# Optimization experiments

Hardware: AMD Instinct MI355X
Metric: run time of the kernel (lower is better)

## Reference

```python
import jax, jax.numpy as jnp
import numpy as np

B, C_IN, H, W = 16, 3, 128, 128
HID = 256      # backbone hidden channels
NC = 21        # num_classes (CRF tag set)
DN = ('NCHW', 'OIHW', 'NCHW')


def setup_inputs() -> dict:
    key = jax.random.key(0)
    ks = jax.random.split(key, 6)
    return {
        "x": jax.random.normal(ks[0], (B, C_IN, H, W), jnp.float32),
        "conv1_w": jax.random.normal(ks[1], (HID, C_IN, 3, 3), jnp.float32) * 0.05,
        "conv1_b": jnp.zeros((HID,), jnp.float32),
        "conv2_w": jax.random.normal(ks[2], (NC, HID, 1, 1), jnp.float32) * 0.05,
        "conv2_b": jnp.zeros((NC,), jnp.float32),
        "start_trans": jax.random.normal(ks[3], (NC,), jnp.float32) * 0.1,
        "end_trans": jax.random.normal(ks[4], (NC,), jnp.float32) * 0.1,
        "trans": jax.random.normal(ks[5], (NC, NC), jnp.float32) * 0.1,
    }


def _backbone(x, w1, b1, w2, b2):
    h = jax.lax.conv_general_dilated(x, w1, (1, 1), 'SAME', dimension_numbers=DN)
    h = jax.nn.relu(h + b1[None, :, None, None])
    out = jax.lax.conv_general_dilated(h, w2, (1, 1), 'SAME', dimension_numbers=DN)
    return out + b2[None, :, None, None]   # [b, NC, H, W]


def _viterbi_decode(emissions, start, end, trans):
    # emissions: [b, L, C]; mask is all-True (as in the module).
    # Forward max-sum recursion (torchcrf _viterbi_decode semantics).
    score0 = emissions[:, 0] + start            # [b, C]

    def fwd(score, emit_t):
        # score[b, prev] + trans[prev, next] + emit_t[b, next] -> [b, prev, next]
        nxt = score[:, :, None] + trans[None, :, :] + emit_t[:, None, :]
        idx = jnp.argmax(nxt, axis=1).astype(jnp.int32)   # backpointers [b, C]
        return jnp.max(nxt, axis=1), idx

    emits = jnp.swapaxes(emissions[:, 1:], 0, 1)          # [L-1, b, C]
    score, hist = jax.lax.scan(fwd, score0, emits)        # hist: [L-1, b, C]
    score = score + end
    last_tag = jnp.argmax(score, axis=1).astype(jnp.int32)  # [b]

    # Backtrack: tag_t = hist[t][b, tag_{t+1}], t = L-2 .. 0
    def bwd(tag_next, idx_t):
        tag_t = jnp.take_along_axis(idx_t, tag_next[:, None], axis=1)[:, 0]
        return tag_t, tag_t

    _, tags_head = jax.lax.scan(bwd, last_tag, hist, reverse=True)  # [L-1, b]
    tags = jnp.concatenate([tags_head, last_tag[None, :]], axis=0)  # [L, b]
    return jnp.swapaxes(tags, 0, 1)                                  # [b, L]


def reference(x, conv1_w, conv1_b, conv2_w, conv2_b, start_trans, end_trans, trans):
    feats = _backbone(x, conv1_w, conv1_b, conv2_w, conv2_b)  # [b, NC, h, w]
    b, c, h, w = feats.shape
    emissions = feats.reshape(b, c, h * w).transpose(0, 2, 1)  # [b, L, C]
    tags = _viterbi_decode(emissions, start_trans, end_trans, trans)  # [b, L]
    return tags.reshape(b, h, w)
```

## Files before the change

kernel.cpp:

```cpp
#include <hip/hip_runtime.h>
#include <stdint.h>

#define NB 16
#define HH 128
#define WW 128
#define L (HH*WW)
#define CIN 3
#define HID 256
#define NC 21
#define CHUNK 256
#define NCHUNKS (L/CHUNK)
#define T_PER 32
#define NPACK (L/4)

__global__ __launch_bounds__(256) void k_conv(
    const float* __restrict__ x, const float* __restrict__ w1,
    const float* __restrict__ b1, const float* __restrict__ w2,
    const float* __restrict__ b2, float* __restrict__ emT)
{
    __shared__ float xs[CIN*4*WW];
    int tid = threadIdx.x;
    int g  = blockIdx.x * 256 + tid;
    int b  = g >> 14;
    int t0 = (blockIdx.x * 256) & (L-1);
    int y0 = t0 >> 7;
    int dy = tid >> 7;
    int xx = tid & (WW-1);
    int t  = t0 + tid;

    const float* xb = x + (size_t)b * CIN * L;
    for (int i = tid; i < CIN*4*WW; i += 256) {
        int ic  = i >> 9;
        int rem = i & 511;
        int rr  = rem >> 7;
        int cc  = rem & 127;
        int row = y0 - 1 + rr;
        xs[i] = (row >= 0 && row < HH) ? xb[ic*L + (row<<7) + cc] : 0.f;
    }
    __syncthreads();

    double p[27];
    #pragma unroll
    for (int ic = 0; ic < CIN; ++ic) {
        #pragma unroll
        for (int ky = 0; ky < 3; ++ky) {
            #pragma unroll
            for (int kx = 0; kx < 3; ++kx) {
                int xc = xx + kx - 1;
                float v = (xc >= 0 && xc < WW) ? xs[ic*512 + (dy+ky)*128 + xc] : 0.f;
                p[ic*9 + ky*3 + kx] = (double)v;
            }
        }
    }

    double acc[NC];
    #pragma unroll
    for (int c = 0; c < NC; ++c) acc[c] = 0.0;

    #pragma unroll 2
    for (int oc = 0; oc < HID; ++oc) {
        double hv = 0.0;
        #pragma unroll
        for (int j = 0; j < 27; ++j) hv += (double)w1[oc*27 + j] * p[j];
        float h32 = (float)hv;
        h32 = h32 + b1[oc];
        h32 = fmaxf(h32, 0.f);
        double hd = (double)h32;
        #pragma unroll
        for (int c = 0; c < NC; ++c) acc[c] += (double)w2[c*HID + oc] * hd;
    }
    float* dstb = emT + (size_t)b * NC * L;
    #pragma unroll
    for (int c = 0; c < NC; ++c) {
        float e32 = (float)acc[c];
        dstb[(size_t)c * L + t] = e32 + b2[c];
    }
}

#define NEGINF (-__builtin_huge_valf())

__global__ __launch_bounds__(64) void k_scores(
    const float* __restrict__ emT, const float* __restrict__ start,
    const float* __restrict__ endt, const float* __restrict__ trans,
    float* __restrict__ sc, int* __restrict__ last_tag)
{
    __shared__ float smem[128];
    __shared__ float fin[NC];
    int l = threadIdx.x;
    int b = blockIdx.x;
    int c = l / 21; if (c > 2) c = 2;
    int n = l - c*21; if (n > 20) n = 20;
    int wb = 8*c;

    const float4* er4 = (const float4*)(emT + ((size_t)b * NC + n) * L);
    float*        scp = sc + (size_t)b * NC * L;

    float tc0, tc1, tc2, tc3, tc4, tc5, tc6, tc7;
    {
        int p0=wb, p1=wb+1, p2=wb+2, p3=wb+3, p4=wb+4, p5=wb+5, p6=wb+6, p7=wb+7;
        tc0 = trans[p0*NC + n];
        tc1 = trans[p1*NC + n];
        tc2 = trans[p2*NC + n];
        tc3 = trans[p3*NC + n];
        tc4 = trans[p4*NC + n];
        tc5 = (p5 < NC) ? trans[p5*NC + n] : NEGINF;
        tc6 = (p6 < NC) ? trans[p6*NC + n] : NEGINF;
        tc7 = (p7 < NC) ? trans[p7*NC + n] : NEGINF;
    }
    asm volatile("" : "+v"(tc0), "+v"(tc1), "+v"(tc2), "+v"(tc3));
    asm volatile("" : "+v"(tc4), "+v"(tc5), "+v"(tc6), "+v"(tc7));

    #define STEP(CUR, NXT, EV, RB) { \
        RB = smem[(CUR)*64 + l];                            \
        smem[(NXT)*64 + l] = NEGINF;                        \
        float4 ra  = *(const float4*)&smem[(CUR)*64 + wb]; \
        float4 rb4 = *(const float4*)&smem[(CUR)*64 + wb + 4]; \
        float w0 = ra.x  + tc0, w1 = ra.y  + tc1, w2 = ra.z  + tc2, w3 = ra.w  + tc3; \
        float w4 = rb4.x + tc4, w5 = rb4.y + tc5, w6 = rb4.z + tc6, w7 = rb4.w + tc7; \
        float m0 = fmaxf(fmaxf(w0, w1), w2); \
        float m1 = fmaxf(fmaxf(w3, w4), w5); \
        float m2 = fmaxf(w6, w7); \
        float q  = fmaxf(fmaxf(m0, m1), m2) + (EV);         \
        (void)__hip_atomic_fetch_max(&smem[(NXT)*64 + n], q, \
                 __ATOMIC_RELAXED, __HIP_MEMORY_SCOPE_WORKGROUP);  \
    }

    float4 ebuf0 = er4[0];
    float4 ebuf1 = er4[1];

    float v0 = ebuf0.x + start[n];
    smem[l] = (l < NC) ? v0 : NEGINF;
    float p0 = v0, p1, p2;
    {
        float4 ev = ebuf0;
        ebuf0 = er4[2];
        float rbB, rbC, rbD;
        STEP(0, 1, ev.y, rbB)
        STEP(1, 0, ev.z, rbC)
        STEP(0, 1, ev.w, rbD)
        (void)rbB;
        p1 = rbC; p2 = rbD;
    }

    for (int k = 1; k < NPACK; ++k) {
        float4 ev = (k & 1) ? ebuf1 : ebuf0;
        int kp = k + 2; if (kp > NPACK-1) kp = NPACK-1;
        if (k & 1) ebuf1 = er4[kp]; else ebuf0 = er4[kp];

        float rbA, rbB, rbC, rbD;
        STEP(1, 0, ev.x, rbA)
        if (l < NC) *(float4*)(scp + (k-1)*84 + n*4) = make_float4(p0, p1, p2, rbA);
        STEP(0, 1, ev.y, rbB)
        STEP(1, 0, ev.z, rbC)
        STEP(0, 1, ev.w, rbD)
        p0 = rbB; p1 = rbC; p2 = rbD;
    }
    #undef STEP

    float slast = smem[64 + l];
    if (l < NC) {
        *(float4*)(scp + (NPACK-1)*84 + n*4) = make_float4(p0, p1, p2, slast);
        fin[n] = slast;
    }
    __syncthreads();
    if (l == 0) {
        float bv = fin[0] + endt[0]; int bt = 0;
        #pragma unroll
        for (int j = 1; j < NC; ++j) {
            float v = fin[j] + endt[j];
            if (v > bv) { bv = v; bt = j; }
        }
        last_tag[b] = bt;
    }
}

__global__ __launch_bounds__(256) void k_bp(
    const float* __restrict__ emT, const float* __restrict__ sc,
    const float* __restrict__ trans, uint8_t* __restrict__ bp)
{
    int wave = threadIdx.x >> 6;
    int lane = threadIdx.x & 63;
    int ne   = lane < NC ? lane : NC-1;

    int bidx  = blockIdx.x;
    int b     = bidx >> 7;
    int tbase = (bidx & 127) * (4*T_PER) + wave*T_PER;

    const float* emb = emT + (size_t)b * NC * L;
    const float* scp = sc  + (size_t)b * NC * L;
    uint8_t*     bpb = bp  + (size_t)b * L * NC;

    float tc[NC];
    #pragma unroll
    for (int pp = 0; pp < NC; ++pp) tc[pp] = trans[pp*NC + ne];

    for (int t = tbase; t < tbase + T_PER; ++t) {
        if (t == 0) continue;
        float target = scp[(t>>2)*84 + ne*4 + (t&3)];
        float e      = emb[(size_t)ne * L + t];
        const float* sp = scp + ((t-1)>>2)*84 + ((t-1)&3);
        int fi = 0;
        #pragma unroll
        for (int pp = NC-1; pp >= 0; --pp) {
            float cand = (sp[pp*4] + tc[pp]) + e;
            if (cand == target) fi = pp;
        }
        if (lane < NC) bpb[(size_t)t * NC + ne] = (uint8_t)fi;
    }
}

__global__ __launch_bounds__(64) void k_jump(
    const uint8_t* __restrict__ bp, uint8_t* __restrict__ J)
{
    __shared__ uint32_t lds4[CHUNK*NC/4];
    __shared__ uint8_t  segJ[8*NC];
    int l   = threadIdx.x;
    int bid = blockIdx.x;
    int b   = bid / (NCHUNKS-1);
    int k   = bid % (NCHUNKS-1) + 1;
    int cs  = k * CHUNK;

    const uint32_t* src = (const uint32_t*)(bp + (size_t)b * L * NC + (size_t)cs * NC);
    for (int i = l; i < CHUNK*NC/4; i += 64) lds4[i] = src[i];
    __syncthreads();
    const uint8_t* lb = (const uint8_t*)lds4;

    int c0 = l, c1 = l + 63, c2 = l + 126;
    bool v2 = (c2 < 8*NC);
    int t0 = c0 % NC, t1 = c1 % NC, t2 = v2 ? (c2 % NC) : 0;
    int r0 = (c0 / NC) * 32, r1 = (c1 / NC) * 32, r2 = v2 ? (c2 / NC) * 32 : 0;
    for (int i = 31; i >= 0; --i) {
        t0 = lb[(r0+i)*NC + t0];
        t1 = lb[(r1+i)*NC + t1];
        if (v2) t2 = lb[(r2+i)*NC + t2];
    }
    segJ[c0] = (uint8_t)t0;
    segJ[c1] = (uint8_t)t1;
    if (v2) segJ[c2] = (uint8_t)t2;
    __syncthreads();

    if (l < NC) {
        int tag = l;
        #pragma unroll
        for (int s = 7; s >= 0; --s) tag = segJ[s*NC + tag];
        J[((size_t)b * NCHUNKS + k) * NC + l] = (uint8_t)tag;
    }
}

__global__ __launch_bounds__(64) void k_seq(
    const uint8_t* __restrict__ J, const int* __restrict__ last_tag,
    uint8_t* __restrict__ ent)
{
    __shared__ uint32_t ldsJ4[NB*NCHUNKS*NC/4];
    int l = threadIdx.x;
    const uint32_t* src = (const uint32_t*)J;
    for (int i = l; i < NB*NCHUNKS*NC/4; i += 64) ldsJ4[i] = src[i];
    __syncthreads();
    const uint8_t* lj = (const uint8_t*)ldsJ4;

    if (l < NB) {
        int b = l;
        int tag = last_tag[b];
        ent[b * NCHUNKS + 63] = (uint8_t)tag;
        for (int k = NCHUNKS-1; k >= 1; --k) {
            tag = lj[((size_t)b * NCHUNKS + k) * NC + tag];
            ent[b * NCHUNKS + (k-1)] = (uint8_t)tag;
        }
    }
}

__global__ __launch_bounds__(64) void k_out(
    const uint8_t* __restrict__ bp, const uint8_t* __restrict__ ent,
    int* __restrict__ out)
{
    __shared__ uint32_t lds4[CHUNK*NC/4];
    __shared__ uint8_t  segJ[8*NC];
    __shared__ uint8_t  E[8];
    __shared__ int      tags[CHUNK];
    int l   = threadIdx.x;
    int bid = blockIdx.x;
    int b   = bid >> 6;
    int k   = bid & (NCHUNKS-1);
    int cs  = k * CHUNK;

    const uint32_t* src = (const uint32_t*)(bp + (size_t)b * L * NC + (size_t)cs * NC);
    for (int i = l; i < CHUNK*NC/4; i += 64) lds4[i] = src[i];
    __syncthreads();
    const uint8_t* lb = (const uint8_t*)lds4;

    int c0 = l, c1 = l + 63, c2 = l + 126;
    bool v2 = (c2 < 8*NC);
    int t0 = c0 % NC, t1 = c1 % NC, t2 = v2 ? (c2 % NC) : 0;
    int r0 = (c0 / NC) * 32, r1 = (c1 / NC) * 32, r2 = v2 ? (c2 / NC) * 32 : 0;
    for (int i = 31; i >= 0; --i) {
        t0 = lb[(r0+i)*NC + t0];
        t1 = lb[(r1+i)*NC + t1];
        if (v2) t2 = lb[(r2+i)*NC + t2];
    }
    segJ[c0] = (uint8_t)(t0 & 31);
    segJ[c1] = (uint8_t)(t1 & 31);
    if (v2) segJ[c2] = (uint8_t)(t2 & 31);
    __syncthreads();

    if (l == 0) {
        int tag = ent[b * NCHUNKS + k];
        E[7] = (uint8_t)tag;
        #pragma unroll
        for (int s = 7; s >= 1; --s) { tag = segJ[s*NC + tag]; E[s-1] = (uint8_t)tag; }
    }
    __syncthreads();

    if (l < 8) {
        int tag = E[l];
        int rb  = l * 32;
        for (int i = 31; i >= 0; --i) {
            tags[rb + i] = tag;
            tag = lb[(rb+i)*NC + tag];
        }
    }
    __syncthreads();

    int4* ob = (int4*)(out + (size_t)b * L + cs);
    ob[l] = ((const int4*)tags)[l];
}

extern "C" void kernel_launch(void* const* d_in, const int* in_sizes, int n_in,
                              void* d_out, int out_size, void* d_ws, size_t ws_size,
                              hipStream_t stream) {
    const float* x  = (const float*)d_in[0];
    const float* w1 = (const float*)d_in[1];
    const float* b1 = (const float*)d_in[2];
    const float* w2 = (const float*)d_in[3];
    const float* b2 = (const float*)d_in[4];
    const float* st = (const float*)d_in[5];
    const float* en = (const float*)d_in[6];
    const float* tr = (const float*)d_in[7];
    int* out = (int*)d_out;

    char* ws = (char*)d_ws;
    float*   em = (float*)ws;
    float*   sc = (float*)(ws + (size_t)NB*L*NC*4);
    uint8_t* bp = (uint8_t*)(ws + (size_t)NB*L*NC*8);
    int*     lt = (int*)(ws + (size_t)NB*L*NC*9);
    uint8_t* J   = (uint8_t*)ws;
    uint8_t* ent = (uint8_t*)ws + 21504;

    k_conv  <<<dim3(NB*L/256),       dim3(256), 0, stream>>>(x, w1, b1, w2, b2, em);
    k_scores<<<dim3(NB),             dim3(64),  0, stream>>>(em, st, en, tr, sc, lt);
    k_bp    <<<dim3(NB*128),         dim3(256), 0, stream>>>(em, sc, tr, bp);
    k_jump  <<<dim3(NB*(NCHUNKS-1)), dim3(64),  0, stream>>>(bp, J);
    k_seq   <<<dim3(1),              dim3(64),  0, stream>>>(J, lt, ent);
    k_out   <<<dim3(NB*NCHUNKS),     dim3(64),  0, stream>>>(bp, ent, out);
}
```

Measured before the change: 1.995 ms.

## Replace LDS atomic max in Viterbi scan with per-partition partial slots

The serial forward scan kernel previously combined the three lane-groups' partial maxima with a workgroup-scope atomic max into shared memory, plus an extra NEGINF reset store each step. Now each lane writes its partial result to a dedicated slot (3 slots per tag), and every lane reads 24 floats and reduces them itself, recovering its own tag's full score through a select tree. This removes the atomic read-modify-write and the reset store from the latency-critical recurrence. In exchange each step does more LDS reads (six float4) and more ALU work, and a padded layout with NEGINF filler slots is needed.

```diff
diff --git a/kernel.cpp b/kernel.cpp
--- a/kernel.cpp
+++ b/kernel.cpp
@@ -84,13 +84,18 @@
     const float* __restrict__ endt, const float* __restrict__ trans,
     float* __restrict__ sc, int* __restrict__ last_tag)
 {
-    __shared__ float smem[128];
+    __shared__ float smem[144];
     __shared__ float fin[NC];
     int l = threadIdx.x;
     int b = blockIdx.x;
     int c = l / 21; if (c > 2) c = 2;
     int n = l - c*21; if (n > 20) n = 20;
-    int wb = 8*c;
+    int wb  = 8*c;
+    int wb3 = 24*c;
+    int wslot = 3*n + c;
+    int ju = n - wb;
+    int j  = ju & 7;
+    bool do_store = ((unsigned)ju < 8u) && (l != 63);
 
     const float4* er4 = (const float4*)(emT + ((size_t)b * NC + n) * L);
     float*        scp = sc + (size_t)b * NC * L;
@@ -110,36 +115,54 @@
     asm volatile("" : "+v"(tc0), "+v"(tc1), "+v"(tc2), "+v"(tc3));
     asm volatile("" : "+v"(tc4), "+v"(tc5), "+v"(tc6), "+v"(tc7));
 
-    #define STEP(CUR, NXT, EV, RB) { \
-        RB = smem[(CUR)*64 + l];                            \
-        smem[(NXT)*64 + l] = NEGINF;                        \
-        float4 ra  = *(const float4*)&smem[(CUR)*64 + wb]; \
-        float4 rb4 = *(const float4*)&smem[(CUR)*64 + wb + 4]; \
-        float w0 = ra.x  + tc0, w1 = ra.y  + tc1, w2 = ra.z  + tc2, w3 = ra.w  + tc3; \
-        float w4 = rb4.x + tc4, w5 = rb4.y + tc5, w6 = rb4.z + tc6, w7 = rb4.w + tc7; \
-        float m0 = fmaxf(fmaxf(w0, w1), w2); \
-        float m1 = fmaxf(fmaxf(w3, w4), w5); \
-        float m2 = fmaxf(w6, w7); \
-        float q  = fmaxf(fmaxf(m0, m1), m2) + (EV);         \
-        (void)__hip_atomic_fetch_max(&smem[(NXT)*64 + n], q, \
-                 __ATOMIC_RELAXED, __HIP_MEMORY_SCOPE_WORKGROUP);  \
+    #define STEP(CUR, NXT, EV, SEL) { \
+        const float* bp_ = &smem[(CUR)*72 + wb3]; \
+        float4 r0 = *(const float4*)(bp_+0); \
+        float4 r1 = *(const float4*)(bp_+4); \
+        float4 r2 = *(const float4*)(bp_+8); \
+        float4 r3 = *(const float4*)(bp_+12); \
+        float4 r4 = *(const float4*)(bp_+16); \
+        float4 r5 = *(const float4*)(bp_+20); \
+        float s0 = fmaxf(fmaxf(r0.x, r0.y), r0.z);    \
+        float s1 = fmaxf(fmaxf(r0.w, r1.x), r1.y); \
+        float s2 = fmaxf(fmaxf(r1.z, r1.w), r2.x); \
+        float s3 = fmaxf(fmaxf(r2.y, r2.z), r2.w); \
+        float s4 = fmaxf(fmaxf(r3.x, r3.y), r3.z); \
+        float s5 = fmaxf(fmaxf(r3.w, r4.x), r4.y); \
+        float s6 = fmaxf(fmaxf(r4.z, r4.w), r5.x); \
+        float s7 = fmaxf(fmaxf(r5.y, r5.z), r5.w); \
+        float x01 = (j&1) ? s1 : s0; \
+        float x23 = (j&1) ? s3 : s2; \
+        float x45 = (j&1) ? s5 : s4; \
+        float x67 = (j&1) ? s7 : s6; \
+        float y0  = (j&2) ? x23 : x01; \
+        float y1  = (j&2) ? x67 : x45; \
+        SEL = (j&4) ? y1 : y0;                        \
+        float w0 = s0+tc0, w1 = s1+tc1, w2 = s2+tc2, w3 = s3+tc3; \
+        float w4 = s4+tc4, w5 = s5+tc5, w6 = s6+tc6, w7 = s7+tc7; \
+        float m0 = fmaxf(fmaxf(w0,w1),w2); \
+        float m1 = fmaxf(fmaxf(w3,w4),w5); \
+        float m2 = fmaxf(w6,w7); \
+        float q  = fmaxf(fmaxf(m0,m1),m2) + (EV);     \
+        smem[(NXT)*72 + wslot] = q; \
     }
 
     float4 ebuf0 = er4[0];
     float4 ebuf1 = er4[1];
 
     float v0 = ebuf0.x + start[n];
-    smem[l] = (l < NC) ? v0 : NEGINF;
+    smem[wslot] = v0;
+    if (l < 9) { smem[63 + l] = NEGINF; smem[135 + l] = NEGINF; }
     float p0 = v0, p1, p2;
     {
         float4 ev = ebuf0;
         ebuf0 = er4[2];
-        float rbB, rbC, rbD;
-        STEP(0, 1, ev.y, rbB)
-        STEP(1, 0, ev.z, rbC)
-        STEP(0, 1, ev.w, rbD)
-        (void)rbB;
-        p1 = rbC; p2 = rbD;
+        float selB, selC, selD;
+        STEP(0, 1, ev.y, selB)
+        STEP(1, 0, ev.z, selC)
+        STEP(0, 1, ev.w, selD)
+        (void)selB;
+        p1 = selC; p2 = selD;
     }
 
     for (int k = 1; k < NPACK; ++k) {
@@ -147,18 +170,42 @@
         int kp = k + 2; if (kp > NPACK-1) kp = NPACK-1;
         if (k & 1) ebuf1 = er4[kp]; else ebuf0 = er4[kp];
 
-        float rbA, rbB, rbC, rbD;
-        STEP(1, 0, ev.x, rbA)
-        if (l < NC) *(float4*)(scp + (k-1)*84 + n*4) = make_float4(p0, p1, p2, rbA);
-        STEP(0, 1, ev.y, rbB)
-        STEP(1, 0, ev.z, rbC)
-        STEP(0, 1, ev.w, rbD)
-        p0 = rbB; p1 = rbC; p2 = rbD;
+        float selA, selB, selC, selD;
+        STEP(1, 0, ev.x, selA)
+        if (do_store) *(float4*)(scp + (k-1)*84 + n*4) = make_float4(p0, p1, p2, selA);
+        STEP(0, 1, ev.y, selB)
+        STEP(1, 0, ev.z, selC)
+        STEP(0, 1, ev.w, selD)
+        p0 = selB; p1 = selC; p2 = selD;
     }
     #undef STEP
 
-    float slast = smem[64 + l];
-    if (l < NC) {
+    float slast;
+    {
+        const float* bp_ = &smem[72 + wb3];
+        float4 r0 = *(const float4*)(bp_+0);
+        float4 r1 = *(const float4*)(bp_+4);
+        float4 r2 = *(const float4*)(bp_+8);
+        float4 r3 = *(const float4*)(bp_+12);
+        float4 r4 = *(const float4*)(bp_+16);
+        float4 r5 = *(const float4*)(bp_+20);
+        float s0 = fmaxf(fmaxf(r0.x, r0.y), r0.z);
+        float s1 = fmaxf(fmaxf(r0.w, r1.x), r1.y);
+        float s2 = fmaxf(fmaxf(r1.z, r1.w), r2.x);
+        float s3 = fmaxf(fmaxf(r2.y, r2.z), r2.w);
+        float s4 = fmaxf(fmaxf(r3.x, r3.y), r3.z);
+        float s5 = fmaxf(fmaxf(r3.w, r4.x), r4.y);
+        float s6 = fmaxf(fmaxf(r4.z, r4.w), r5.x);
+        float s7 = fmaxf(fmaxf(r5.y, r5.z), r5.w);
+        float x01 = (j&1) ? s1 : s0;
+        float x23 = (j&1) ? s3 : s2;
+        float x45 = (j&1) ? s5 : s4;
+        float x67 = (j&1) ? s7 : s6;
+        float y0  = (j&2) ? x23 : x01;
+        float y1  = (j&2) ? x67 : x45;
+        slast = (j&4) ? y1 : y0;
+    }
+    if (do_store) {
         *(float4*)(scp + (NPACK-1)*84 + n*4) = make_float4(p0, p1, p2, slast);
         fin[n] = slast;
     }
@@ -166,9 +213,9 @@
     if (l == 0) {
         float bv = fin[0] + endt[0]; int bt = 0;
         #pragma unroll
-        for (int j = 1; j < NC; ++j) {
-            float v = fin[j] + endt[j];
-            if (v > bv) { bv = v; bt = j; }
+        for (int jj = 1; jj < NC; ++jj) {
+            float v = fin[jj] + endt[jj];
+            if (v > bv) { bv = v; bt = jj; }
         }
         last_tag[b] = bt;
     }
```

Measured after the change: 2.585 ms. 29.6% more time.
